# Kernel tuning notes

Hardware: AMD Instinct MI355X
Metric: run time of the kernel (lower is better)

The kernel has to match this reference:

```python
import jax, jax.numpy as jnp
import numpy as np

EPS = 1e-6        # module eps added to softplus(sigma)
BALL_EPS = 1e-5   # clip margin for Poincare ball projection


def _norm(x):
    return jnp.sqrt(jnp.clip(jnp.sum(x * x, axis=-1, keepdims=True), 1e-15))


def _clip_norm(x, max_norm):
    n = _norm(x)
    return x * jnp.minimum(1.0, max_norm / n)


def _artanh(x):
    return jnp.arctanh(jnp.clip(x, -1.0 + 1e-7, 1.0 - 1e-7))


def _expmap0(u, c):
    """pre_clip -> PoincareBall.expmap0 -> post_clip."""
    sc = jnp.sqrt(c)
    max_tan = jnp.arctanh(jnp.asarray(1.0 - BALL_EPS, u.dtype)) / sc
    u = _clip_norm(u, max_tan)                      # pre_clip on tangent norm
    n = _norm(u)
    y = jnp.tanh(sc * n) * u / (sc * n)
    return _clip_norm(y, (1.0 - BALL_EPS) / sc)     # post_clip inside ball


def _logmap0(y, c):
    sc = jnp.sqrt(c)
    n = _norm(y)
    return _artanh(sc * n) * y / (sc * n)


def _pair_dist(qh, kh, c):
    """Poincare distance d(q_i, k_j) computed from inner products (no [B,H,N,J,D] tensor).
    qh: (B,H,N,D), kh: (B,H,J,D) -> (B,H,N,J).
    d = (2/sqrt(c)) * artanh(sqrt(c) * ||(-q) mobius_add k||).
    """
    x2 = jnp.sum(qh * qh, -1)[..., :, None]   # (B,H,N,1)
    y2 = jnp.sum(kh * kh, -1)[..., None, :]   # (B,H,1,J)
    xy = jnp.einsum('bhnd,bhjd->bhnj', qh, kh)
    A = 1.0 - 2.0 * c * xy + c * y2
    Bc = 1.0 - c * x2
    num2 = A * A * x2 - 2.0 * A * Bc * xy + Bc * Bc * y2   # ||numerator||^2
    den = 1.0 - 2.0 * c * xy + (c * c) * x2 * y2
    arg = jnp.sqrt(c) * jnp.sqrt(jnp.clip(num2, 0.0)) / jnp.clip(den, 1e-15)
    return (2.0 / jnp.sqrt(c)) * _artanh(arg)


def _mobius_scalar_mul(r, x, c):
    sc = jnp.sqrt(c)
    n = _norm(x)
    return jnp.tanh(r * _artanh(sc * n)) * x / (sc * n)


def setup_inputs() -> dict:
    key = jax.random.key(0)
    ks = jax.random.split(key, 8)
    B, N, D, H, M = 16, 576, 768, 12, 128
    Hd = D // H
    std = 0.02
    isp1 = float(np.log(np.expm1(1.0)))  # inv_softplus(1.0)
    return {
        'x': jax.random.normal(ks[0], (B, N, D), jnp.float32),
        'Wq': jax.random.normal(ks[1], (D, D), jnp.float32) * std,
        'bq': jnp.zeros((D,), jnp.float32),
        'Wk': jax.random.normal(ks[2], (D, D), jnp.float32) * std,
        'bk': jnp.zeros((D,), jnp.float32),
        'Wv': jax.random.normal(ks[3], (D, D), jnp.float32) * std,
        'bv': jnp.zeros((D,), jnp.float32),
        'Wo': jax.random.normal(ks[4], (D, D), jnp.float32) * std,
        'bo': jnp.zeros((D,), jnp.float32),
        'centroids': jax.random.normal(ks[5], (H, M, Hd), jnp.float32) * std,
        'curv_raw': jnp.full((1,), isp1, jnp.float32),
        'sigma_raw': jnp.full((H,), isp1, jnp.float32),
    }


def reference(x, Wq, bq, Wk, bk, Wv, bv, Wo, bo, centroids, curv_raw, sigma_raw):
    B, N, D = x.shape
    H, M, Hd = centroids.shape
    c = jax.nn.softplus(curv_raw[0])

    def split(t):  # (B,N,D) -> (B,H,N,Hd)
        return t.reshape(B, N, H, Hd).transpose(0, 2, 1, 3)

    q = split(x @ Wq.T + bq)
    k = split(x @ Wk.T + bk)
    v = split(x @ Wv.T + bv)

    Cb = jnp.broadcast_to(centroids[None], (B, H, M, Hd))
    K_aug = jnp.concatenate([k, Cb], axis=2)   # (B,H,J,Hd), J = N + M
    V_aug = jnp.concatenate([v, Cb], axis=2)

    q_h = _expmap0(q, c)
    K_h = _expmap0(K_aug, c)
    V_h = _expmap0(V_aug, c)

    d = _pair_dist(q_h, K_h, c)                              # (B,H,N,J)
    sigma = (jax.nn.softplus(sigma_raw) + EPS)[None, :, None, None]
    W = jax.nn.softmax(-(d * d) / (2.0 * sigma * sigma), axis=-1)

    # Riemannian weighted midpoint (geoopt weighted_midpoint with k=-c):
    # gamma = lambda_x = 2 / (1 - c||x||^2)
    gamma = 2.0 / jnp.clip(1.0 - c * jnp.sum(V_h * V_h, -1), 1e-15)  # (B,H,J)
    nom = jnp.einsum('bhnj,bhjd->bhnd', W * gamma[:, :, None, :], V_h)
    den = jnp.einsum('bhnj,bhj->bhn', W, gamma - 1.0)
    den = jnp.where(den >= 0, jnp.maximum(den, 1e-10), jnp.minimum(den, -1e-10))
    two_mean = nom / den[..., None]
    O_h = _mobius_scalar_mul(0.5, two_mean, c)
    O_euc = _logmap0(O_h, c)                                  # (B,H,N,Hd)

    out = O_euc.transpose(0, 2, 1, 3).reshape(B, N, H * Hd)
    return out @ Wo.T + bo
```

## Files before the change

### kernel.cpp

```cpp
#include <hip/hip_runtime.h>
#include <cstdint>
#include <cstddef>

#define B_  16
#define N_  576
#define D_  768
#define H_  12
#define HD_ 64
#define M_  128
#define J_  704

typedef unsigned short u16;
typedef __attribute__((ext_vector_type(8))) short bf16x8;
typedef __attribute__((ext_vector_type(4))) float f32x4;
typedef __attribute__((ext_vector_type(4))) unsigned short u16x4;
typedef __attribute__((ext_vector_type(8))) unsigned short u16x8;


__device__ __forceinline__ float softplus_f(float x) {
    return (x > 20.f) ? x : log1pf(expf(x));
}

__device__ __forceinline__ float wred_sum64(float v) {
#pragma unroll
    for (int m = 1; m < 64; m <<= 1) v += __shfl_xor(v, m, 64);
    return v;
}

__device__ __forceinline__ u16 bf16_rne(float f) {
    unsigned int u = __float_as_uint(f);
    unsigned int r = u + 0x7FFFu + ((u >> 16) & 1u);
    return (u16)(r >> 16);
}
__device__ __forceinline__ float bf16_tof(u16 h) {
    return __uint_as_float(((unsigned int)h) << 16);
}

__device__ __forceinline__ float expmap0_factor(float n2, float sc, float* n2out) {
    const float ATANH_1M1E5 = 6.1030335f;
    const float LOG2E2 = 2.8853900817779268f;
    float rsc = __builtin_amdgcn_rcpf(sc);
    float n0 = __builtin_amdgcn_sqrtf(fmaxf(n2, 1e-15f));
    float f1 = fminf(1.f, (ATANH_1M1E5 * rsc) * __builtin_amdgcn_rcpf(n0));
    float n1 = n0 * f1;
    float a  = sc * n1;
    float e2a = __builtin_amdgcn_exp2f(a * LOG2E2);
    float th  = 1.f - 2.f * __builtin_amdgcn_rcpf(e2a + 1.f);
    float yfac  = th * __builtin_amdgcn_rcpf(a);
    float f2 = fminf(1.f, 0.99999f * __builtin_amdgcn_rcpf(th));
    float fn = (th * rsc) * f2;
    *n2out = fn * fn;
    return f1 * yfac * f2;
}

__device__ __forceinline__ float artanh_fast(float z) {
    return 0.5f * __logf((1.f + z) / (1.f - z));
}

typedef const __attribute__((address_space(1))) unsigned int* gas_u32;
typedef __attribute__((address_space(3))) unsigned int* las_u32;
__device__ __forceinline__ void gload_lds16(const u16* g, u16* l) {
    __builtin_amdgcn_global_load_lds((gas_u32)(const void*)g, (las_u32)(void*)l, 16, 0, 0);
}

__global__ __launch_bounds__(256) void split_bf16_kernel(
    const float* __restrict__ src, u16* __restrict__ hi, u16* __restrict__ lo, int n4)
{
    int i = blockIdx.x * 256 + threadIdx.x;
    if (i >= n4) return;
    float4 v = ((const float4*)src)[i];
    u16x4 h, l;
    h[0] = bf16_rne(v.x); l[0] = bf16_rne(v.x - bf16_tof(h[0]));
    h[1] = bf16_rne(v.y); l[1] = bf16_rne(v.y - bf16_tof(h[1]));
    h[2] = bf16_rne(v.z); l[2] = bf16_rne(v.z - bf16_tof(h[2]));
    h[3] = bf16_rne(v.w); l[3] = bf16_rne(v.w - bf16_tof(h[3]));
    ((u16x4*)hi)[i] = h;
    ((u16x4*)lo)[i] = l;
}

__global__ __launch_bounds__(256) void split_w4_kernel(
    const float* __restrict__ W0, const float* __restrict__ W1,
    const float* __restrict__ W2, const float* __restrict__ W3,
    u16* __restrict__ H0, u16* __restrict__ L0, u16* __restrict__ H1, u16* __restrict__ L1,
    u16* __restrict__ H2, u16* __restrict__ L2, u16* __restrict__ H3, u16* __restrict__ L3)
{
    int i = blockIdx.x * 256 + threadIdx.x;
    const int wsel = blockIdx.y;
    const float* src = wsel == 0 ? W0 : (wsel == 1 ? W1 : (wsel == 2 ? W2 : W3));
    u16* hi = wsel == 0 ? H0 : (wsel == 1 ? H1 : (wsel == 2 ? H2 : H3));
    u16* lo = wsel == 0 ? L0 : (wsel == 1 ? L1 : (wsel == 2 ? L2 : L3));
    float4 v = ((const float4*)src)[i];
    u16x4 h, l;
    h[0] = bf16_rne(v.x); l[0] = bf16_rne(v.x - bf16_tof(h[0]));
    h[1] = bf16_rne(v.y); l[1] = bf16_rne(v.y - bf16_tof(h[1]));
    h[2] = bf16_rne(v.z); l[2] = bf16_rne(v.z - bf16_tof(h[2]));
    h[3] = bf16_rne(v.w); l[3] = bf16_rne(v.w - bf16_tof(h[3]));
    ((u16x4*)hi)[i] = h;
    ((u16x4*)lo)[i] = l;
}

__global__ __launch_bounds__(256) void gemm_qkv_mfma(
    const u16* __restrict__ xh, const u16* __restrict__ xl,
    const u16* __restrict__ Wh0, const u16* __restrict__ Wl0,
    const u16* __restrict__ Wh1, const u16* __restrict__ Wl1,
    const u16* __restrict__ Wh2, const u16* __restrict__ Wl2,
    const float* __restrict__ bq, const float* __restrict__ bk, const float* __restrict__ bv,
    u16* __restrict__ Qb0, u16* __restrict__ Qb1, u16* __restrict__ Qb2,
    u16* __restrict__ Kb0, u16* __restrict__ Kb1, u16* __restrict__ Kb2,
    u16* __restrict__ gV0, u16* __restrict__ gV1,
    float* __restrict__ x2q, float* __restrict__ y2g, float* __restrict__ gm1,
    float* __restrict__ rbj,
    const float* __restrict__ curv_raw)
{
    __shared__ u16 Ah[2][4096], Al[2][4096], Bh[2][4096], Bl[2][4096];
    const int tid = threadIdx.x;
    const int w = tid >> 6, lane = tid & 63;
    const int wr = w >> 1, wc = w & 1;
    const int lrow = lane & 15, lk8 = (lane >> 4) << 3;
    const int lg = lane >> 4;
    const int bid = blockIdx.x;
    const int xcd = bid & 7, ser = bid >> 3;
    const int mt = xcd * 9 + (ser % 9);
    const int yb = ser / 9;
    const int which = yb / 6, ct = yb - which * 6;
    const u16* Bp_h = which == 0 ? Wh0 : (which == 1 ? Wh1 : Wh2);
    const u16* Bp_l = which == 0 ? Wl0 : (which == 1 ? Wl1 : Wl2);
    const int row0 = mt * 128, col0 = ct * 128;

    const size_t a0 = (size_t)(row0 + (2 * w + 0) * 16 + lrow) * 768 + lk8;
    const size_t a1 = a0 + 16 * 768;
    const size_t b0 = (size_t)(col0 + (2 * w + 0) * 16 + lrow) * 768 + lk8;
    const size_t b1 = b0 + 16 * 768;
    const int wo = (2 * w) * 512;

    auto STAGE = [&](int k0, int buf) {
        gload_lds16(xh + a0 + k0, &Ah[buf][wo]);
        gload_lds16(xh + a1 + k0, &Ah[buf][wo + 512]);
        gload_lds16(xl + a0 + k0, &Al[buf][wo]);
        gload_lds16(xl + a1 + k0, &Al[buf][wo + 512]);
        gload_lds16(Bp_h + b0 + k0, &Bh[buf][wo]);
        gload_lds16(Bp_h + b1 + k0, &Bh[buf][wo + 512]);
        gload_lds16(Bp_l + b0 + k0, &Bl[buf][wo]);
        gload_lds16(Bp_l + b1 + k0, &Bl[buf][wo + 512]);
    };

    f32x4 acc[4][4];
#pragma unroll
    for (int i = 0; i < 4; ++i)
#pragma unroll
        for (int j = 0; j < 4; ++j) acc[i][j] = (f32x4){0.f, 0.f, 0.f, 0.f};

    STAGE(0, 0);
    asm volatile("s_waitcnt vmcnt(0)" ::: "memory");
    __builtin_amdgcn_sched_barrier(0);
    __builtin_amdgcn_s_barrier();
    __builtin_amdgcn_sched_barrier(0);

    const int lo8 = lane * 8;
    int cur = 0;
    for (int k0 = 0; k0 < 768; k0 += 32) {
        if (k0 < 736) {
            STAGE(k0 + 32, cur ^ 1);
            asm volatile("s_waitcnt vmcnt(8)" ::: "memory");
        } else {
            asm volatile("s_waitcnt vmcnt(0)" ::: "memory");
        }
        __builtin_amdgcn_sched_barrier(0);
        __builtin_amdgcn_s_barrier();
        __builtin_amdgcn_sched_barrier(0);
        bf16x8 aH[4], aL[4], bH[4], bL[4];
#pragma unroll
        for (int i = 0; i < 4; ++i) {
            aH[i] = *(const bf16x8*)(&Ah[cur][(wr * 4 + i) * 512 + lo8]);
            aL[i] = *(const bf16x8*)(&Al[cur][(wr * 4 + i) * 512 + lo8]);
            bH[i] = *(const bf16x8*)(&Bh[cur][(wc * 4 + i) * 512 + lo8]);
            bL[i] = *(const bf16x8*)(&Bl[cur][(wc * 4 + i) * 512 + lo8]);
        }
#pragma unroll
        for (int mi = 0; mi < 4; ++mi)
#pragma unroll
            for (int ni = 0; ni < 4; ++ni) {
                acc[mi][ni] = __builtin_amdgcn_mfma_f32_16x16x32_bf16(aH[mi], bH[ni], acc[mi][ni], 0, 0, 0);
                acc[mi][ni] = __builtin_amdgcn_mfma_f32_16x16x32_bf16(aH[mi], bL[ni], acc[mi][ni], 0, 0, 0);
                acc[mi][ni] = __builtin_amdgcn_mfma_f32_16x16x32_bf16(aL[mi], bH[ni], acc[mi][ni], 0, 0, 0);
            }
        __builtin_amdgcn_sched_barrier(0);
        __builtin_amdgcn_s_barrier();
        __builtin_amdgcn_sched_barrier(0);
        cur ^= 1;
    }

    const float* bias = which == 0 ? bq : (which == 1 ? bk : bv);
    const int h = ct * 2 + wc;
    const int rbase = row0 + wr * 64 + (lg << 2);
    const float c  = softplus_f(curv_raw[0]);
    const float sc = sqrtf(c);
    float bvv[4];
#pragma unroll
    for (int ni = 0; ni < 4; ++ni) bvv[ni] = bias[h * 64 + ni * 16 + lrow];

#pragma unroll
    for (int mi = 0; mi < 4; ++mi) {
        float v4[4][4];
#pragma unroll
        for (int ni = 0; ni < 4; ++ni) {
            f32x4 a = acc[mi][ni];
#pragma unroll
            for (int r = 0; r < 4; ++r) v4[ni][r] = a[r] + bvv[ni];
        }
        float f_[4], n2o_[4];
#pragma unroll
        for (int r = 0; r < 4; ++r) {
            float s = v4[0][r] * v4[0][r];
#pragma unroll
            for (int ni = 1; ni < 4; ++ni) s = fmaf(v4[ni][r], v4[ni][r], s);
#pragma unroll
            for (int m = 1; m < 16; m <<= 1) s += __shfl_xor(s, m, 64);
            f_[r] = expmap0_factor(s, sc, &n2o_[r]);
        }
        const int row0g = rbase + mi * 16;
        const int bb = row0g / 576;
        const int nn0 = row0g - bb * 576;
        const size_t gbase = ((size_t)(bb * 12 + h)) * 576 + nn0;
        if (which == 2) {
            float gmm[4];
#pragma unroll
            for (int r = 0; r < 4; ++r)
                gmm[r] = 2.f * __builtin_amdgcn_rcpf(fmaxf(1.f - c * n2o_[r], 1e-15f));
            if (lrow == 0) {
#pragma unroll
                for (int r = 0; r < 4; ++r) gm1[gbase + r] = gmm[r] - 1.f;
            }
#pragma unroll
            for (int ni = 0; ni < 4; ++ni) {
                const int hd = ni * 16 + lrow;
                u16x4 hs, ls;
#pragma unroll
                for (int r = 0; r < 4; ++r) {
                    float gv = v4[ni][r] * f_[r] * gmm[r];
                    u16 hb = bf16_rne(gv);
                    hs[r] = hb;
                    ls[r] = bf16_rne(gv - bf16_tof(hb));
                }
                const size_t dst = (((size_t)(bb * 12 + h)) * 64 + hd) * 576 + nn0;
                *(u16x4*)(gV0 + dst) = hs;
                *(u16x4*)(gV1 + dst) = ls;
            }
        } else {
            float* scal = which == 0 ? x2q : y2g;
            if (lrow == 0) {
#pragma unroll
                for (int r = 0; r < 4; ++r) scal[gbase + r] = n2o_[r];
                if (which == 1) {
#pragma unroll
                    for (int r = 0; r < 4; ++r)
                        rbj[gbase + r] = __builtin_amdgcn_rcpf(fmaf(-c, n2o_[r], 1.f));
                }
            }
            u16* P0 = which == 0 ? Qb0 : Kb0;
            u16* P1 = which == 0 ? Qb1 : Kb1;
            u16* P2 = which == 0 ? Qb2 : Kb2;
#pragma unroll
            for (int ni = 0; ni < 4; ++ni) {
                const int hd = ni * 16 + lrow;
#pragma unroll
                for (int r = 0; r < 4; ++r) {
                    float y = v4[ni][r] * f_[r];
                    u16 hb = bf16_rne(y);
                    float r1 = y - bf16_tof(hb);
                    u16 mb = bf16_rne(r1);
                    u16 lb2 = bf16_rne(r1 - bf16_tof(mb));
                    const size_t off = (gbase + r) * 64 + hd;
                    P0[off] = hb; P1[off] = mb; P2[off] = lb2;
                }
            }
        }
    }
}

__global__ __launch_bounds__(256) void gemm_o_mfma(
    const u16* __restrict__ Oh, const u16* __restrict__ Ol,
    const u16* __restrict__ Wh, const u16* __restrict__ Wl,
    const float* __restrict__ bo, float* __restrict__ out)
{
    __shared__ u16 Ah[2][4096], Al[2][4096], Bh[2][4096], Bl[2][4096];
    const int tid = threadIdx.x;
    const int w = tid >> 6, lane = tid & 63;
    const int wr = w >> 1, wc = w & 1;
    const int lrow = lane & 15, lk8 = (lane >> 4) << 3;
    const int bid = blockIdx.x;
    const int xcd = bid & 7, ser = bid >> 3;
    const int mt = xcd * 9 + (ser % 9);
    const int ct = ser / 9;
    const int row0 = mt * 128, col0 = ct * 128;

    const size_t a0 = (size_t)(row0 + (2 * w + 0) * 16 + lrow) * 768 + lk8;
    const size_t a1 = a0 + 16 * 768;
    const size_t b0 = (size_t)(col0 + (2 * w + 0) * 16 + lrow) * 768 + lk8;
    const size_t b1 = b0 + 16 * 768;
    const int wo = (2 * w) * 512;

    auto STAGE = [&](int k0, int buf) {
        gload_lds16(Oh + a0 + k0, &Ah[buf][wo]);
        gload_lds16(Oh + a1 + k0, &Ah[buf][wo + 512]);
        gload_lds16(Ol + a0 + k0, &Al[buf][wo]);
        gload_lds16(Ol + a1 + k0, &Al[buf][wo + 512]);
        gload_lds16(Wh + b0 + k0, &Bh[buf][wo]);
        gload_lds16(Wh + b1 + k0, &Bh[buf][wo + 512]);
        gload_lds16(Wl + b0 + k0, &Bl[buf][wo]);
        gload_lds16(Wl + b1 + k0, &Bl[buf][wo + 512]);
    };

    f32x4 acc[4][4];
#pragma unroll
    for (int i = 0; i < 4; ++i)
#pragma unroll
        for (int j = 0; j < 4; ++j) acc[i][j] = (f32x4){0.f, 0.f, 0.f, 0.f};

    STAGE(0, 0);
    asm volatile("s_waitcnt vmcnt(0)" ::: "memory");
    __builtin_amdgcn_sched_barrier(0);
    __builtin_amdgcn_s_barrier();
    __builtin_amdgcn_sched_barrier(0);

    const int lo8 = lane * 8;
    int cur = 0;
    for (int k0 = 0; k0 < 768; k0 += 32) {
        if (k0 < 736) {
            STAGE(k0 + 32, cur ^ 1);
            asm volatile("s_waitcnt vmcnt(8)" ::: "memory");
        } else {
            asm volatile("s_waitcnt vmcnt(0)" ::: "memory");
        }
        __builtin_amdgcn_sched_barrier(0);
        __builtin_amdgcn_s_barrier();
        __builtin_amdgcn_sched_barrier(0);
        bf16x8 aH[4], aL[4], bH[4], bL[4];
#pragma unroll
        for (int i = 0; i < 4; ++i) {
            aH[i] = *(const bf16x8*)(&Ah[cur][(wr * 4 + i) * 512 + lo8]);
            aL[i] = *(const bf16x8*)(&Al[cur][(wr * 4 + i) * 512 + lo8]);
            bH[i] = *(const bf16x8*)(&Bh[cur][(wc * 4 + i) * 512 + lo8]);
            bL[i] = *(const bf16x8*)(&Bl[cur][(wc * 4 + i) * 512 + lo8]);
        }
#pragma unroll
        for (int mi = 0; mi < 4; ++mi)
#pragma unroll
            for (int ni = 0; ni < 4; ++ni) {
                acc[mi][ni] = __builtin_amdgcn_mfma_f32_16x16x32_bf16(aH[mi], bH[ni], acc[mi][ni], 0, 0, 0);
                acc[mi][ni] = __builtin_amdgcn_mfma_f32_16x16x32_bf16(aH[mi], bL[ni], acc[mi][ni], 0, 0, 0);
                acc[mi][ni] = __builtin_amdgcn_mfma_f32_16x16x32_bf16(aL[mi], bH[ni], acc[mi][ni], 0, 0, 0);
            }
        __builtin_amdgcn_sched_barrier(0);
        __builtin_amdgcn_s_barrier();
        __builtin_amdgcn_sched_barrier(0);
        cur ^= 1;
    }

    const int rbase = row0 + wr * 64 + ((lane >> 4) << 2);
#pragma unroll
    for (int ni = 0; ni < 4; ++ni) {
        const int colg = col0 + wc * 64 + ni * 16 + lrow;
        const float bv_ = bo[colg];
#pragma unroll
        for (int mi = 0; mi < 4; ++mi) {
            f32x4 a = acc[mi][ni];
#pragma unroll
            for (int r = 0; r < 4; ++r) {
                int row = rbase + mi * 16 + r;
                out[(size_t)row * 768 + colg] = a[r] + bv_;
            }
        }
    }
}

__global__ __launch_bounds__(256) void cent_kernel(
    const float* __restrict__ cent,
    u16* __restrict__ Kc0, u16* __restrict__ Kc1, u16* __restrict__ Kc2,
    u16* __restrict__ gVc0, u16* __restrict__ gVc1,
    float* __restrict__ y2c, float* __restrict__ gm1c, float* __restrict__ rbc,
    const float* __restrict__ curv_raw)
{
    __shared__ float gvt_s[64][65];
    const float c  = softplus_f(curv_raw[0]);
    const float sc = sqrtf(c);
    const int t = blockIdx.x;
    const int h = t >> 1, ct = t & 1;
    const int w = threadIdx.x >> 6, lane = threadIdx.x & 63;
#pragma unroll 4
    for (int i = 0; i < 16; ++i) {
        const int m = ct * 64 + w * 16 + i;
        const size_t g = (size_t)h * 128 + m;
        float cv = cent[g * 64 + lane];
        float n2 = wred_sum64(cv * cv);
        float n2o;
        float f = expmap0_factor(n2, sc, &n2o);
        float ky = cv * f;
        u16 kh = bf16_rne(ky);
        float r1 = ky - bf16_tof(kh);
        u16 km = bf16_rne(r1);
        u16 kl = bf16_rne(r1 - bf16_tof(km));
        Kc0[g * 64 + lane] = kh; Kc1[g * 64 + lane] = km; Kc2[g * 64 + lane] = kl;
        float gmm = 2.f * __builtin_amdgcn_rcpf(fmaxf(1.f - c * n2o, 1e-15f));
        gvt_s[lane][w * 16 + i] = ky * gmm;
        if (lane == 0) {
            y2c[g] = n2o; gm1c[g] = gmm - 1.f;
            rbc[g] = __builtin_amdgcn_rcpf(fmaf(-c, n2o, 1.f));
        }
    }
    __syncthreads();
    const int hd = threadIdx.x >> 2, j0 = (threadIdx.x & 3) * 16;
    u16 hb[16], lb[16];
#pragma unroll
    for (int e = 0; e < 16; ++e) {
        float v = gvt_s[hd][j0 + e];
        hb[e] = bf16_rne(v);
        lb[e] = bf16_rne(v - bf16_tof(hb[e]));
    }
    const size_t dst = ((size_t)h * 64 + hd) * 128 + ct * 64 + j0;
    *(u16x8*)(gVc0 + dst)     = *(u16x8*)&hb[0];
    *(u16x8*)(gVc0 + dst + 8) = *(u16x8*)&hb[8];
    *(u16x8*)(gVc1 + dst)     = *(u16x8*)&lb[0];
    *(u16x8*)(gVc1 + dst + 8) = *(u16x8*)&lb[8];
}

__global__ __launch_bounds__(256) void attn_kernel(
    const u16* __restrict__ Qb0, const u16* __restrict__ Qb1, const u16* __restrict__ Qb2,
    const u16* __restrict__ Kb0, const u16* __restrict__ Kb1, const u16* __restrict__ Kb2,
    const u16* __restrict__ Kc0, const u16* __restrict__ Kc1, const u16* __restrict__ Kc2,
    const u16* __restrict__ gV0, const u16* __restrict__ gV1,
    const u16* __restrict__ gVc0, const u16* __restrict__ gVc1,
    const float* __restrict__ x2q, const float* __restrict__ y2g, const float* __restrict__ gm1,
    const float* __restrict__ y2c, const float* __restrict__ gm1c,
    const float* __restrict__ rbj, const float* __restrict__ rbc,
    const float* __restrict__ sigma_raw, const float* __restrict__ curv_raw,
    u16* __restrict__ Oh, u16* __restrict__ Ol)
{
    __shared__ __align__(16) u16 Kst[2][3][4096];
    __shared__ __align__(16) u16 Vst[2][4096];
    __shared__ __align__(16) u16 wb_hi[4][1024];
    __shared__ __align__(16) u16 wb_lo[4][1024];

    const int blk = blockIdx.x;
    const int xcd = blk & 7;
    const int serial = blk >> 3;
    const int bhg = serial / 9;
    const int qt = serial - bhg * 9;
    const int bh = bhg * 8 + xcd;
    const int b = bh / 12, h = bh % 12;
    const float c  = softplus_f(curv_raw[0]);
    const float sc = sqrtf(c);
    const float sig = softplus_f(sigma_raw[h]) + 1e-6f;
    const float coef = -2.f / (c * sig * sig);
    const float c2h  = coef * 0.25f * 0.6931471805599453f;

    const int tid = threadIdx.x;
    const int w = tid >> 6, lane = tid & 63;
    const int lr = lane & 15, lg = lane >> 4, lo8 = lg * 8;
    const int swl = (lr & 7) << 3;

    const size_t qbase = (size_t)bh * 576 + qt * 64;

    int srow[2], scol[2];
#pragma unroll
    for (int rr = 0; rr < 2; ++rr) {
        int cch = (rr * 4 + w) * 64 + lane;
        srow[rr] = cch >> 3;
        scol[rr] = ((cch & 7) ^ (srow[rr] & 7)) << 3;
    }
    const size_t kb_base = (size_t)bh * 576 * 64;
    const size_t kc_base = (size_t)h * 128 * 64;
    const size_t vb_base = (size_t)bh * 64 * 576;
    const size_t vc_base = (size_t)h * 64 * 128;

    auto stageK = [&](int t, int buf) {
        if (t < 9) {
            const size_t rb = kb_base + (size_t)t * 64 * 64;
#pragma unroll
            for (int rr = 0; rr < 2; ++rr) {
                const size_t so = rb + (size_t)srow[rr] * 64 + scol[rr];
                gload_lds16(Kb0 + so, &Kst[buf][0][(rr * 4 + w) * 512]);
                gload_lds16(Kb1 + so, &Kst[buf][1][(rr * 4 + w) * 512]);
                gload_lds16(Kb2 + so, &Kst[buf][2][(rr * 4 + w) * 512]);
            }
        } else {
            const size_t rb = kc_base + (size_t)(t - 9) * 64 * 64;
#pragma unroll
            for (int rr = 0; rr < 2; ++rr) {
                const size_t so = rb + (size_t)srow[rr] * 64 + scol[rr];
                gload_lds16(Kc0 + so, &Kst[buf][0][(rr * 4 + w) * 512]);
                gload_lds16(Kc1 + so, &Kst[buf][1][(rr * 4 + w) * 512]);
                gload_lds16(Kc2 + so, &Kst[buf][2][(rr * 4 + w) * 512]);
            }
        }
    };
    auto stageV = [&](int t) {
        if (t < 9) {
            const size_t rb = vb_base + (size_t)t * 64;
#pragma unroll
            for (int rr = 0; rr < 2; ++rr) {
                const size_t so = rb + (size_t)srow[rr] * 576 + scol[rr];
                gload_lds16(gV0 + so, &Vst[0][(rr * 4 + w) * 512]);
                gload_lds16(gV1 + so, &Vst[1][(rr * 4 + w) * 512]);
            }
        } else {
            const size_t rb = vc_base + (size_t)(t - 9) * 64;
#pragma unroll
            for (int rr = 0; rr < 2; ++rr) {
                const size_t so = rb + (size_t)srow[rr] * 128 + scol[rr];
                gload_lds16(gVc0 + so, &Vst[0][(rr * 4 + w) * 512]);
                gload_lds16(gVc1 + so, &Vst[1][(rr * 4 + w) * 512]);
            }
        }
    };

    bf16x8 aQh[2], aQm[2], aQl[2];
    {
        const size_t qrow = (qbase + w * 16 + lr) * 64;
#pragma unroll
        for (int kt = 0; kt < 2; ++kt) {
            const size_t o = qrow + kt * 32 + lo8;
            aQh[kt] = *(const bf16x8*)(Qb0 + o);
            aQm[kt] = *(const bf16x8*)(Qb1 + o);
            aQl[kt] = *(const bf16x8*)(Qb2 + o);
        }
    }
    float x2r[4], Pr[4];
#pragma unroll
    for (int r = 0; r < 4; ++r) {
        float x2 = x2q[qbase + w * 16 + lg * 4 + r];
        x2r[r] = x2;
        Pr[r] = (c + c) / fmaf(-c, x2, 1.f);
    }

    f32x4 pv[4];
#pragma unroll
    for (int i = 0; i < 4; ++i) pv[i] = (f32x4){0.f, 0.f, 0.f, 0.f};
    float den[4] = {0.f, 0.f, 0.f, 0.f};

    u16* wbh = &wb_hi[w][0];
    u16* wbl = &wb_lo[w][0];

    stageK(0, 0);
    __syncthreads();

    int cur = 0;
    for (int jt = 0; jt < 11; ++jt) {
        const int jb = jt * 64;

        if (jt < 10) stageK(jt + 1, cur ^ 1);
        stageV(jt);

        const float* y2p;
        const float* gm1p;
        const float* rbp;
        if (jt < 9) {
            y2p = y2g + (size_t)bh * 576 + jb;  gm1p = gm1 + (size_t)bh * 576 + jb;
            rbp = rbj + (size_t)bh * 576 + jb;
        } else {
            y2p = y2c + (size_t)h * 128 + (jb - 576); gm1p = gm1c + (size_t)h * 128 + (jb - 576);
            rbp = rbc + (size_t)h * 128 + (jb - 576);
        }

        const u16* kp0 = &Kst[cur][0][0];
        const u16* kp1 = &Kst[cur][1][0];
        const u16* kp2 = &Kst[cur][2][0];
        f32x4 sf[4];
        float y2v[4], gm1v[4], rbv[4];
#pragma unroll
        for (int jf = 0; jf < 4; ++jf) {
            y2v[jf] = y2p[jf * 16 + lr];
            gm1v[jf] = gm1p[jf * 16 + lr];
            rbv[jf] = rbp[jf * 16 + lr];
            const int rb = (jf * 16 + lr) * 64;
            f32x4 s = (f32x4){0.f, 0.f, 0.f, 0.f};
#pragma unroll
            for (int kt = 0; kt < 2; ++kt) {
                const int o = rb + ((kt * 32 + lo8) ^ swl);
                bf16x8 kh = *(const bf16x8*)(kp0 + o);
                bf16x8 km = *(const bf16x8*)(kp1 + o);
                bf16x8 kl = *(const bf16x8*)(kp2 + o);
                s = __builtin_amdgcn_mfma_f32_16x16x32_bf16(aQh[kt], kh, s, 0, 0, 0);
                s = __builtin_amdgcn_mfma_f32_16x16x32_bf16(aQh[kt], km, s, 0, 0, 0);
                s = __builtin_amdgcn_mfma_f32_16x16x32_bf16(aQm[kt], kh, s, 0, 0, 0);
                s = __builtin_amdgcn_mfma_f32_16x16x32_bf16(aQm[kt], km, s, 0, 0, 0);
                s = __builtin_amdgcn_mfma_f32_16x16x32_bf16(aQh[kt], kl, s, 0, 0, 0);
                s = __builtin_amdgcn_mfma_f32_16x16x32_bf16(aQl[kt], kh, s, 0, 0, 0);
            }
            sf[jf] = s;
        }

#pragma unroll
        for (int jf = 0; jf < 4; ++jf) {
            const float y2 = y2v[jf];
            const float rb_ = rbv[jf];
#pragma unroll
            for (int r = 0; r < 4; ++r) {
                float xy = sf[jf][r];
                float sxy = x2r[r] + y2;
                float u = fmaf(-2.f, xy, sxy);
                float krr = Pr[r] * rb_;
                float z = fmaxf(fmaf(krr, u, 1.f), 1.f);
                float zm = fmaxf(fmaf(z, z, -1.f), 0.f);
                float lg2 = __builtin_amdgcn_logf(z + __builtin_amdgcn_sqrtf(zm));
                float wv_ = __builtin_amdgcn_exp2f(c2h * (lg2 * lg2));
                sf[jf][r] = wv_;
                den[r] = fmaf(wv_, gm1v[jf], den[r]);
            }
        }

#pragma unroll
        for (int r = 0; r < 4; ++r) {
            const int row = lg * 4 + r;
            const int sw = (row & 7) << 3;
#pragma unroll
            for (int jf = 0; jf < 4; ++jf) {
                const int colu = (jf * 16 + lr) ^ sw;
                float wv_ = sf[jf][r];
                u16 hb = bf16_rne(wv_);
                wbh[row * 64 + colu] = hb;
                wbl[row * 64 + colu] = bf16_rne(wv_ - bf16_tof(hb));
            }
        }

        __syncthreads();

        bf16x8 aWh[2], aWl[2];
#pragma unroll
        for (int kt = 0; kt < 2; ++kt) {
            const int colu = (kt * 32 + lo8) ^ swl;
            aWh[kt] = *(const bf16x8*)(wbh + lr * 64 + colu);
            aWl[kt] = *(const bf16x8*)(wbl + lr * 64 + colu);
        }

#pragma unroll
        for (int hf = 0; hf < 4; ++hf) {
            const int rb = (hf * 16 + lr) * 64;
#pragma unroll
            for (int kt = 0; kt < 2; ++kt) {
                const int o = rb + ((kt * 32 + lo8) ^ swl);
                bf16x8 vh = *(const bf16x8*)(&Vst[0][o]);
                bf16x8 vl = *(const bf16x8*)(&Vst[1][o]);
                pv[hf] = __builtin_amdgcn_mfma_f32_16x16x32_bf16(aWh[kt], vh, pv[hf], 0, 0, 0);
                pv[hf] = __builtin_amdgcn_mfma_f32_16x16x32_bf16(aWh[kt], vl, pv[hf], 0, 0, 0);
                pv[hf] = __builtin_amdgcn_mfma_f32_16x16x32_bf16(aWl[kt], vh, pv[hf], 0, 0, 0);
            }
        }

        __syncthreads();
        cur ^= 1;
    }

#pragma unroll
    for (int r = 0; r < 4; ++r) {
        float d = den[r];
#pragma unroll
        for (int msk = 1; msk < 16; msk <<= 1) d += __shfl_xor(d, msk, 64);
        float rd = 1.f / d;
        float o_[4];
        float n2 = 0.f;
#pragma unroll
        for (int hf = 0; hf < 4; ++hf) { o_[hf] = pv[hf][r] * rd; n2 = fmaf(o_[hf], o_[hf], n2); }
#pragma unroll
        for (int msk = 1; msk < 16; msk <<= 1) n2 += __shfl_xor(n2, msk, 64);
        float nrm = sqrtf(fmaxf(n2, 1e-15f));
        float arg = fminf(sc * nrm, 1.f - 1e-7f);
        float t = artanh_fast(arg);
        float f = 0.5f * t / (sc * nrm);
        const int nrow = qt * 64 + w * 16 + lg * 4 + r;
        const size_t dst = ((size_t)(b * 576 + nrow)) * 768 + h * 64;
#pragma unroll
        for (int hf = 0; hf < 4; ++hf) {
            float val = o_[hf] * f;
            u16 hb = bf16_rne(val);
            Oh[dst + hf * 16 + lr] = hb;
            Ol[dst + hf * 16 + lr] = bf16_rne(val - bf16_tof(hb));
        }
    }
}

extern "C" void kernel_launch(void* const* d_in, const int* in_sizes, int n_in,
                              void* d_out, int out_size, void* d_ws, size_t ws_size,
                              hipStream_t stream) {
    (void)in_sizes; (void)n_in; (void)out_size; (void)ws_size;
    const float* x    = (const float*)d_in[0];
    const float* Wq   = (const float*)d_in[1];
    const float* bq   = (const float*)d_in[2];
    const float* Wk   = (const float*)d_in[3];
    const float* bk   = (const float*)d_in[4];
    const float* Wv   = (const float*)d_in[5];
    const float* bv   = (const float*)d_in[6];
    const float* Wo   = (const float*)d_in[7];
    const float* bo   = (const float*)d_in[8];
    const float* cent = (const float*)d_in[9];
    const float* curv = (const float*)d_in[10];
    const float* sigr = (const float*)d_in[11];
    float* out = (float*)d_out;

    const size_t QH  = (size_t)B_ * H_ * N_ * 64;
    const size_t CK  = (size_t)H_ * M_ * 64;
    const size_t WSZ = (size_t)D_ * D_;

    float* fp = (float*)d_ws;
    float* x2q  = fp;            fp += (size_t)B_ * H_ * N_;
    float* y2g  = fp;            fp += (size_t)B_ * H_ * N_;
    float* gm1  = fp;            fp += (size_t)B_ * H_ * N_;
    float* rbjv = fp;            fp += (size_t)B_ * H_ * N_;
    float* y2c  = fp;            fp += (size_t)H_ * M_;
    float* gm1c = fp;            fp += (size_t)H_ * M_;
    float* rbcv = fp;            fp += (size_t)H_ * M_;
    u16* up = (u16*)fp;
    u16* xh  = up;  up += QH;
    u16* xl  = up;  up += QH;
    u16* Oh  = xh;
    u16* Ol  = xl;
    u16* Wqh = up;  up += WSZ;
    u16* Wql = up;  up += WSZ;
    u16* Wkh = up;  up += WSZ;
    u16* Wkl = up;  up += WSZ;
    u16* Wvh = up;  up += WSZ;
    u16* Wvl = up;  up += WSZ;
    u16* Woh = up;  up += WSZ;
    u16* Wol = up;  up += WSZ;
    u16* Qb  = up;  up += 3 * QH;
    u16* Kb  = up;  up += 3 * QH;
    u16* gV  = up;  up += 2 * QH;
    u16* Kc  = up;  up += 3 * CK;
    u16* gVc = up;  up += 2 * CK;

    u16* Qb0 = Qb;           u16* Qb1 = Qb + QH;   u16* Qb2 = Qb + 2 * QH;
    u16* Kb0 = Kb;           u16* Kb1 = Kb + QH;   u16* Kb2 = Kb + 2 * QH;
    u16* gV0 = gV;           u16* gV1 = gV + QH;
    u16* Kc0 = Kc;           u16* Kc1 = Kc + CK;   u16* Kc2 = Kc + 2 * CK;
    u16* gVc0 = gVc;         u16* gVc1 = gVc + CK;

    split_bf16_kernel<<<(int)(QH / 4 / 256), 256, 0, stream>>>(x, xh, xl, (int)(QH / 4));
    split_w4_kernel<<<dim3((int)(WSZ / 4 / 256), 4), 256, 0, stream>>>(
        Wq, Wk, Wv, Wo, Wqh, Wql, Wkh, Wkl, Wvh, Wvl, Woh, Wol);

    cent_kernel<<<24, 256, 0, stream>>>(cent, Kc0, Kc1, Kc2, gVc0, gVc1, y2c, gm1c, rbcv, curv);

    gemm_qkv_mfma<<<1296, 256, 0, stream>>>(xh, xl, Wqh, Wql, Wkh, Wkl, Wvh, Wvl,
                                            bq, bk, bv,
                                            Qb0, Qb1, Qb2, Kb0, Kb1, Kb2, gV0, gV1,
                                            x2q, y2g, gm1, rbjv, curv);
    attn_kernel<<<1728, 256, 0, stream>>>(Qb0, Qb1, Qb2, Kb0, Kb1, Kb2, Kc0, Kc1, Kc2,
                                          gV0, gV1, gVc0, gVc1,
                                          x2q, y2g, gm1, y2c, gm1c, rbjv, rbcv,
                                          sigr, curv, Oh, Ol);
    gemm_o_mfma<<<432, 256, 0, stream>>>(Oh, Ol, Woh, Wol, bo, out);
}
```

Measured before the change: 371.8 us.

## Drop K double-buffer and V LDS staging to raise attention occupancy

The K tile is now single-buffered in LDS and V fragments are read straight from global memory instead of being staged through LDS. Launch bounds ask for 4 blocks per SM. This shrinks shared memory per block so more blocks can be resident, trading away the overlap between loading the next K tile and computing on the current one. The direct global V loads skip LDS swizzling and may be less coalesced or have higher latency. Removing the barrier between the W writes and reads relies on each wave reading only its own wb rows.

Result: slower. 622.5 us (+67.5%).

```diff
diff --git a/kernel.cpp b/kernel.cpp
--- a/kernel.cpp
+++ b/kernel.cpp
@@ -424,7 +424,7 @@
     *(u16x8*)(gVc1 + dst + 8) = *(u16x8*)&lb[8];
 }
 
-__global__ __launch_bounds__(256) void attn_kernel(
+__global__ __launch_bounds__(256, 4) void attn_kernel(
     const u16* __restrict__ Qb0, const u16* __restrict__ Qb1, const u16* __restrict__ Qb2,
     const u16* __restrict__ Kb0, const u16* __restrict__ Kb1, const u16* __restrict__ Kb2,
     const u16* __restrict__ Kc0, const u16* __restrict__ Kc1, const u16* __restrict__ Kc2,
@@ -436,8 +436,7 @@
     const float* __restrict__ sigma_raw, const float* __restrict__ curv_raw,
     u16* __restrict__ Oh, u16* __restrict__ Ol)
 {
-    __shared__ __align__(16) u16 Kst[2][3][4096];
-    __shared__ __align__(16) u16 Vst[2][4096];
+    __shared__ __align__(16) u16 Kst[3][4096];
     __shared__ __align__(16) u16 wb_hi[4][1024];
     __shared__ __align__(16) u16 wb_lo[4][1024];
 
@@ -470,46 +469,25 @@
     }
     const size_t kb_base = (size_t)bh * 576 * 64;
     const size_t kc_base = (size_t)h * 128 * 64;
-    const size_t vb_base = (size_t)bh * 64 * 576;
-    const size_t vc_base = (size_t)h * 64 * 128;
-
-    auto stageK = [&](int t, int buf) {
+
+    auto stageK = [&](int t) {
         if (t < 9) {
             const size_t rb = kb_base + (size_t)t * 64 * 64;
 #pragma unroll
             for (int rr = 0; rr < 2; ++rr) {
                 const size_t so = rb + (size_t)srow[rr] * 64 + scol[rr];
-                gload_lds16(Kb0 + so, &Kst[buf][0][(rr * 4 + w) * 512]);
-                gload_lds16(Kb1 + so, &Kst[buf][1][(rr * 4 + w) * 512]);
-                gload_lds16(Kb2 + so, &Kst[buf][2][(rr * 4 + w) * 512]);
+                gload_lds16(Kb0 + so, &Kst[0][(rr * 4 + w) * 512]);
+                gload_lds16(Kb1 + so, &Kst[1][(rr * 4 + w) * 512]);
+                gload_lds16(Kb2 + so, &Kst[2][(rr * 4 + w) * 512]);
             }
         } else {
             const size_t rb = kc_base + (size_t)(t - 9) * 64 * 64;
 #pragma unroll
             for (int rr = 0; rr < 2; ++rr) {
                 const size_t so = rb + (size_t)srow[rr] * 64 + scol[rr];
-                gload_lds16(Kc0 + so, &Kst[buf][0][(rr * 4 + w) * 512]);
-                gload_lds16(Kc1 + so, &Kst[buf][1][(rr * 4 + w) * 512]);
-                gload_lds16(Kc2 + so, &Kst[buf][2][(rr * 4 + w) * 512]);
-            }
-        }
-    };
-    auto stageV = [&](int t) {
-        if (t < 9) {
-            const size_t rb = vb_base + (size_t)t * 64;
-#pragma unroll
-            for (int rr = 0; rr < 2; ++rr) {
-                const size_t so = rb + (size_t)srow[rr] * 576 + scol[rr];
-                gload_lds16(gV0 + so, &Vst[0][(rr * 4 + w) * 512]);
-                gload_lds16(gV1 + so, &Vst[1][(rr * 4 + w) * 512]);
-            }
-        } else {
-            const size_t rb = vc_base + (size_t)(t - 9) * 64;
-#pragma unroll
-            for (int rr = 0; rr < 2; ++rr) {
-                const size_t so = rb + (size_t)srow[rr] * 128 + scol[rr];
-                gload_lds16(gVc0 + so, &Vst[0][(rr * 4 + w) * 512]);
-                gload_lds16(gVc1 + so, &Vst[1][(rr * 4 + w) * 512]);
+                gload_lds16(Kc0 + so, &Kst[0][(rr * 4 + w) * 512]);
+                gload_lds16(Kc1 + so, &Kst[1][(rr * 4 + w) * 512]);
+                gload_lds16(Kc2 + so, &Kst[2][(rr * 4 + w) * 512]);
             }
         }
     };
@@ -541,30 +519,35 @@
     u16* wbh = &wb_hi[w][0];
     u16* wbl = &wb_lo[w][0];
 
-    stageK(0, 0);
-    __syncthreads();
-
-    int cur = 0;
     for (int jt = 0; jt < 11; ++jt) {
         const int jb = jt * 64;
 
-        if (jt < 10) stageK(jt + 1, cur ^ 1);
-        stageV(jt);
+        stageK(jt);
+        __syncthreads();
 
         const float* y2p;
         const float* gm1p;
         const float* rbp;
+        const u16* v0p;
+        const u16* v1p;
+        int vstr;
         if (jt < 9) {
             y2p = y2g + (size_t)bh * 576 + jb;  gm1p = gm1 + (size_t)bh * 576 + jb;
             rbp = rbj + (size_t)bh * 576 + jb;
+            v0p = gV0 + (size_t)(bh * 64) * 576 + jb;
+            v1p = gV1 + (size_t)(bh * 64) * 576 + jb;
+            vstr = 576;
         } else {
             y2p = y2c + (size_t)h * 128 + (jb - 576); gm1p = gm1c + (size_t)h * 128 + (jb - 576);
             rbp = rbc + (size_t)h * 128 + (jb - 576);
-        }
-
-        const u16* kp0 = &Kst[cur][0][0];
-        const u16* kp1 = &Kst[cur][1][0];
-        const u16* kp2 = &Kst[cur][2][0];
+            v0p = gVc0 + (size_t)(h * 64) * 128 + (jb - 576);
+            v1p = gVc1 + (size_t)(h * 64) * 128 + (jb - 576);
+            vstr = 128;
+        }
+
+        const u16* kp0 = &Kst[0][0];
+        const u16* kp1 = &Kst[1][0];
+        const u16* kp2 = &Kst[2][0];
         f32x4 sf[4];
         float y2v[4], gm1v[4], rbv[4];
 #pragma unroll
@@ -623,8 +606,6 @@
             }
         }
 
-        __syncthreads();
-
         bf16x8 aWh[2], aWl[2];
 #pragma unroll
         for (int kt = 0; kt < 2; ++kt) {
@@ -635,12 +616,12 @@
 
 #pragma unroll
         for (int hf = 0; hf < 4; ++hf) {
-            const int rb = (hf * 16 + lr) * 64;
+            const size_t vrow = (size_t)(hf * 16 + lr) * vstr;
 #pragma unroll
             for (int kt = 0; kt < 2; ++kt) {
-                const int o = rb + ((kt * 32 + lo8) ^ swl);
-                bf16x8 vh = *(const bf16x8*)(&Vst[0][o]);
-                bf16x8 vl = *(const bf16x8*)(&Vst[1][o]);
+                const size_t o = vrow + kt * 32 + lo8;
+                bf16x8 vh = *(const bf16x8*)(v0p + o);
+                bf16x8 vl = *(const bf16x8*)(v1p + o);
                 pv[hf] = __builtin_amdgcn_mfma_f32_16x16x32_bf16(aWh[kt], vh, pv[hf], 0, 0, 0);
                 pv[hf] = __builtin_amdgcn_mfma_f32_16x16x32_bf16(aWh[kt], vl, pv[hf], 0, 0, 0);
                 pv[hf] = __builtin_amdgcn_mfma_f32_16x16x32_bf16(aWl[kt], vh, pv[hf], 0, 0, 0);
@@ -648,7 +629,6 @@
         }
 
         __syncthreads();
-        cur ^= 1;
     }
 
 #pragma unroll
```
